# Kernel optimization log

Measured on AMD Instinct MI355X. Metric: run time of the kernel, lower is better.

Reference implementation:

```python
import jax, jax.numpy as jnp
import numpy as np

B, S, D, H, M = 4, 1024, 1024, 16, 128
HD = D // H  # 64


def setup_inputs() -> dict:
    key = jax.random.key(0)
    ks = jax.random.split(key, 12)
    s = 0.02
    return {
        "x": jax.random.normal(ks[0], (B, S, D), dtype=jnp.float32),
        "Wq": jax.random.normal(ks[1], (D, D), dtype=jnp.float32) * s,
        "bq": jnp.zeros((D,), dtype=jnp.float32),
        "Wk": jax.random.normal(ks[2], (D, D), dtype=jnp.float32) * s,
        "bk": jnp.zeros((D,), dtype=jnp.float32),
        "Wv": jax.random.normal(ks[3], (D, D), dtype=jnp.float32) * s,
        "bv": jnp.zeros((D,), dtype=jnp.float32),
        "Wo": jax.random.normal(ks[4], (D, D), dtype=jnp.float32) * s,
        "bo": jnp.zeros((D,), dtype=jnp.float32),
        "u": jax.random.normal(ks[5], (H, HD), dtype=jnp.float32) * s,
        "v": jax.random.normal(ks[6], (H, HD), dtype=jnp.float32) * s,
    }


def _rel_sinusoid_emb():
    # [2M+1, HD] sinusoidal embeddings over relative offsets -M..M
    rel_range = jnp.arange(-M, M + 1, dtype=jnp.float32)
    inv_freq = 1.0 / (10000.0 ** (jnp.arange(0, HD, 2, dtype=jnp.float32) / HD))
    sinusoid = rel_range[:, None] * inv_freq[None, :]  # [2M+1, HD/2]
    emb = jnp.zeros((2 * M + 1, HD), dtype=jnp.float32)
    emb = emb.at[:, 0::2].set(jnp.sin(sinusoid))
    emb = emb.at[:, 1::2].set(jnp.cos(sinusoid))
    return emb


def reference(x, Wq, bq, Wk, bk, Wv, bv, Wo, bo, u, v):
    scale = 1.0 / np.sqrt(HD).astype(np.float32)

    def heads(t):  # [B,S,D] -> [B,H,S,HD]
        return t.reshape(B, S, H, HD).transpose(0, 2, 1, 3)

    q = heads(x @ Wq + bq)
    k = heads(x @ Wk + bk)
    vv = heads(x @ Wv + bv)

    rel_emb = _rel_sinusoid_emb()  # [2M+1, HD]
    pos = jnp.arange(S)
    rel_index = jnp.clip(pos[None, :] - pos[:, None], -M, M) + M  # [S,S] int

    q_u = q + u[None, :, None, :]
    q_v = q + v[None, :, None, :]

    content = jnp.einsum("bhid,bhjd->bhij", q_u, k) * scale  # [B,H,S,S]
    # einsum('bhid,ijd->bhij', q_v, rel_emb[rel_index]) == gather of per-bucket scores
    rel_all = jnp.einsum("bhid,rd->bhir", q_v, rel_emb) * scale  # [B,H,S,2M+1]
    rel_scores = jnp.take_along_axis(rel_all, rel_index[None, None, :, :], axis=-1)

    attn = jax.nn.softmax(content + rel_scores, axis=-1)
    out = jnp.einsum("bhij,bhjd->bhid", attn, vv)  # [B,H,S,HD]
    out = out.transpose(0, 2, 1, 3).reshape(B, S, D)
    return out @ Wo + bo
```

## Files before the change

kernel.cpp:

```cpp
#include <hip/hip_runtime.h>
#include <math.h>


#define BB 4
#define SS 1024
#define DD 1024
#define HH 16
#define HDIM 64
#define SCALE 0.125f
#define KMAX_BOUND 16.0f

typedef __attribute__((ext_vector_type(8))) short short8;
typedef __attribute__((ext_vector_type(4))) float f32x4;
typedef __attribute__((ext_vector_type(4))) unsigned short us4;
typedef unsigned short u16;

#define MFMA __builtin_amdgcn_mfma_f32_16x16x32_bf16

__device__ __forceinline__ float b2f(u16 v) {
  return __uint_as_float((unsigned)v << 16);
}
__device__ __forceinline__ u16 f2b(float f) {
  unsigned u = __float_as_uint(f);
  return (u16)((u + 0x7FFF + ((u >> 16) & 1)) >> 16);
}
__device__ __forceinline__ void gl_lds16(const u16* g, u16* l) {
  __builtin_amdgcn_global_load_lds(
      (const __attribute__((address_space(1))) unsigned int*)(g),
      (__attribute__((address_space(3))) unsigned int*)(l), 16, 0, 0);
}

__global__ __launch_bounds__(256) void prep(
    const float* __restrict__ x,
    const float* __restrict__ W0, const float* __restrict__ W1,
    const float* __restrict__ W2, const float* __restrict__ W3,
    u16* __restrict__ xb,
    u16* __restrict__ T0, u16* __restrict__ T1,
    u16* __restrict__ T2, u16* __restrict__ T3,
    u16* __restrict__ Eb) {
  __shared__ float t[64 * 68];
  const int bid = blockIdx.x, tid = threadIdx.x;
  if (bid < 2048) {
    const size_t i = ((size_t)bid * 256 + tid) * 8;
    float4 a = *reinterpret_cast<const float4*>(&x[i]);
    float4 b = *reinterpret_cast<const float4*>(&x[i + 4]);
    short8 v;
    v[0] = (short)f2b(a.x); v[1] = (short)f2b(a.y);
    v[2] = (short)f2b(a.z); v[3] = (short)f2b(a.w);
    v[4] = (short)f2b(b.x); v[5] = (short)f2b(b.y);
    v[6] = (short)f2b(b.z); v[7] = (short)f2b(b.w);
    *reinterpret_cast<short8*>(&xb[i]) = v;
  } else if (bid < 3072) {
    const int wz = bid - 2048;
    const int z = wz >> 8;
    const float* W = z == 0 ? W0 : z == 1 ? W1 : z == 2 ? W2 : W3;
    u16* T = z == 0 ? T0 : z == 1 ? T1 : z == 2 ? T2 : T3;
    const int k0 = ((wz >> 4) & 15) * 64, n0 = (wz & 15) * 64;
#pragma unroll
    for (int rd = 0; rd < 4; ++rd) {
      const int idx = rd * 256 + tid;
      const int r = idx >> 4, c4 = (idx & 15) * 4;
      *reinterpret_cast<float4*>(&t[r * 68 + c4]) =
          *reinterpret_cast<const float4*>(&W[(size_t)(k0 + r) * DD + n0 + c4]);
    }
    __syncthreads();
#pragma unroll
    for (int rd = 0; rd < 2; ++rd) {
      const int idx = rd * 256 + tid;
      const int rr = idx >> 3, cc = (idx & 7) * 8;
      short8 v;
#pragma unroll
      for (int e = 0; e < 8; ++e) v[e] = (short)f2b(t[(cc + e) * 68 + rr]);
      *reinterpret_cast<short8*>(&T[(size_t)(n0 + rr) * DD + k0 + cc]) = v;
    }
  } else {
    const int j = (bid - 3072) * 4 + (tid >> 6);
    const int d = tid & 63;
    const int pair = d >> 1;
    const float inv_freq =
        exp2f(-((float)(2 * pair) / 64.0f) * 13.287712379549449f);
    const float arg = (float)j * inv_freq;
    const float val = (d & 1) ? cosf(arg) : sinf(arg);
    Eb[j * 64 + d] = f2b(val);
  }
}

__global__ __launch_bounds__(256, 3) void gemm_mfma(
    const u16* __restrict__ A,
    const u16* __restrict__ W0, const u16* __restrict__ W1, const u16* __restrict__ W2,
    const float* __restrict__ b0, const float* __restrict__ b1, const float* __restrict__ b2,
    void* o0, void* o1, void* o2, int final_mode) {
  const int z = blockIdx.z;
  const u16* Bt = z == 0 ? W0 : z == 1 ? W1 : W2;
  const float* bias = z == 0 ? b0 : z == 1 ? b1 : b2;
  __shared__ u16 As0[128 * 32];
  __shared__ u16 Bs0[128 * 32];
  __shared__ u16 As1[128 * 32];
  __shared__ u16 Bs1[128 * 32];
  const int tid = threadIdx.x;
  const int bm = blockIdx.y * 128, bn = blockIdx.x * 128;
  const int lane = tid & 63, w = tid >> 6;
  const int wr = w >> 1, wc = w & 1;
  const int lr = lane & 15, lg = lane >> 4;

  const int r_i0 = 32 * w + (lane >> 2);
  const int r_i1 = r_i0 + 16;
  const int q0 = (lane & 3) ^ ((r_i0 >> 1) & 3);
  const int q1 = (lane & 3) ^ ((r_i1 >> 1) & 3);
  const u16* gA0 = &A[(size_t)(bm + r_i0) * DD + q0 * 8];
  const u16* gA1 = &A[(size_t)(bm + r_i1) * DD + q1 * 8];
  const u16* gB0 = &Bt[(size_t)(bn + r_i0) * DD + q0 * 8];
  const u16* gB1 = &Bt[(size_t)(bn + r_i1) * DD + q1 * 8];
  const int lo0 = (32 * w) * 32;
  const int lo1 = (32 * w + 16) * 32;

  const f32x4 Z4 = {0.f, 0.f, 0.f, 0.f};
  f32x4 acc[4][4];
#pragma unroll
  for (int m = 0; m < 4; ++m)
#pragma unroll
    for (int n = 0; n < 4; ++n) acc[m][n] = Z4;

  auto STAGE = [&](u16* Ab, u16* Bb, int kk) {
    gl_lds16(gA0 + kk, Ab + lo0);
    gl_lds16(gA1 + kk, Ab + lo1);
    gl_lds16(gB0 + kk, Bb + lo0);
    gl_lds16(gB1 + kk, Bb + lo1);
  };
  auto COMPUTE = [&](u16* Ab, u16* Bb) {
    short8 af[4], bf[4];
#pragma unroll
    for (int m = 0; m < 4; ++m) {
      const int row = wr * 64 + m * 16 + lr;
      af[m] = *reinterpret_cast<short8*>(&Ab[row * 32 + ((lg ^ ((row >> 1) & 3)) * 8)]);
    }
#pragma unroll
    for (int n = 0; n < 4; ++n) {
      const int row = wc * 64 + n * 16 + lr;
      bf[n] = *reinterpret_cast<short8*>(&Bb[row * 32 + ((lg ^ ((row >> 1) & 3)) * 8)]);
    }
#pragma unroll
    for (int m = 0; m < 4; ++m)
#pragma unroll
      for (int n = 0; n < 4; ++n)
        acc[m][n] = MFMA(af[m], bf[n], acc[m][n], 0, 0, 0);
  };

  STAGE(As0, Bs0, 0);
  __syncthreads();
  for (int k0 = 0; k0 < DD; k0 += 64) {
    STAGE(As1, Bs1, k0 + 32);
    COMPUTE(As0, Bs0);
    __syncthreads();
    if (k0 + 64 < DD) STAGE(As0, Bs0, k0 + 64);
    COMPUTE(As1, Bs1);
    __syncthreads();
  }

  const int mode = final_mode ? 2 : (z == 2 ? 1 : 0);
  u16* ob = (u16*)(z == 0 ? o0 : z == 1 ? o1 : o2);
  float* of = (float*)o0;
#pragma unroll
  for (int m = 0; m < 4; ++m) {
#pragma unroll
    for (int n = 0; n < 4; ++n) {
      const int col = bn + wc * 64 + n * 16 + lr;
      const float bv = bias[col];
      const int row0 = bm + wr * 64 + m * 16 + lg * 4;
      if (mode == 0) {
#pragma unroll
        for (int g = 0; g < 4; ++g)
          ob[(size_t)(row0 + g) * DD + col] = f2b(acc[m][n][g] + bv);
      } else if (mode == 2) {
#pragma unroll
        for (int g = 0; g < 4; ++g)
          of[(size_t)(row0 + g) * DD + col] = acc[m][n][g] + bv;
      } else {
        const int bI = row0 >> 10, s0 = row0 & 1023;
        us4 pk;
#pragma unroll
        for (int g = 0; g < 4; ++g) pk[g] = f2b(acc[m][n][g] + bv);
        *reinterpret_cast<us4*>(&ob[(size_t)col * 4096 + bI * 1024 + s0]) = pk;
      }
    }
  }
}

__global__ __launch_bounds__(256, 2) void attn_mfma(
    const u16* __restrict__ Qg, const u16* __restrict__ Kg,
    const u16* __restrict__ Vtg, const u16* __restrict__ Eb,
    const float* __restrict__ ub, const float* __restrict__ vb,
    u16* __restrict__ AO) {
  __shared__ u16 kk0[64 * 128];
  __shared__ u16 kk1[64 * 128];
  __shared__ u16 vt0[64 * 64];
  __shared__ u16 vt1[64 * 64];
  __shared__ u16 ps_l[128 * 64];
  __shared__ float ls_l[128];

  const int tid = threadIdx.x;
  const int it = blockIdx.x, h = blockIdx.y, b = blockIdx.z;
  const int i0 = it * 128;
  const int lane = tid & 63, w = tid >> 6;
  const int lr = lane & 15, lg = lane >> 4;
  const f32x4 Z4 = {0.f, 0.f, 0.f, 0.f};
  auto needE = [&](int j0) { const int d = j0 - i0; return d >= -191 && d <= 255; };

  short8 aq[2][4];
  float bI[2], bL[2], bR[2];
#pragma unroll
  for (int m = 0; m < 2; ++m) {
    const int qpos = i0 + w * 32 + m * 16 + lr;
    const size_t qbase = (size_t)(b * SS + qpos) * DD + h * 64;
    const int iL = qpos >= 128 ? qpos - 128 : 0;
    const int iR = qpos <= 895 ? qpos + 128 : 1023;
    float nqu = 0.f, nqv = 0.f, clp = 0.f, crp = 0.f;
#pragma unroll
    for (int ks2 = 0; ks2 < 2; ++ks2) {
      const int d8 = ks2 * 32 + lg * 8;
      short8 q8 = *reinterpret_cast<const short8*>(&Qg[qbase + d8]);
      short8 e8 = *reinterpret_cast<const short8*>(&Eb[qpos * 64 + d8]);
      short8 eL8 = *reinterpret_cast<const short8*>(&Eb[iL * 64 + d8]);
      short8 eR8 = *reinterpret_cast<const short8*>(&Eb[iR * 64 + d8]);
      float us[8], vs[8];
      {
        float4 a = *reinterpret_cast<const float4*>(&ub[h * 64 + d8]);
        float4 d = *reinterpret_cast<const float4*>(&ub[h * 64 + d8 + 4]);
        us[0] = a.x; us[1] = a.y; us[2] = a.z; us[3] = a.w;
        us[4] = d.x; us[5] = d.y; us[6] = d.z; us[7] = d.w;
        float4 e = *reinterpret_cast<const float4*>(&vb[h * 64 + d8]);
        float4 f = *reinterpret_cast<const float4*>(&vb[h * 64 + d8 + 4]);
        vs[0] = e.x; vs[1] = e.y; vs[2] = e.z; vs[3] = e.w;
        vs[4] = f.x; vs[5] = f.y; vs[6] = f.z; vs[7] = f.w;
      }
      short8 xu, xr;
#pragma unroll
      for (int e = 0; e < 8; ++e) {
        const float qf = b2f((u16)q8[e]);
        xu[e] = (short)f2b(qf + us[e]);
        const float quf = b2f((u16)xu[e]);
        nqu = fmaf(quf, quf, nqu);
      }
#pragma unroll
      for (int p = 0; p < 4; ++p) {
        const float qv0 = b2f((u16)q8[2 * p]) + vs[2 * p];
        const float qv1 = b2f((u16)q8[2 * p + 1]) + vs[2 * p + 1];
        const float si = b2f((u16)e8[2 * p]), co = b2f((u16)e8[2 * p + 1]);
        const float r0 = qv0 * co + qv1 * si;
        const float r1 = qv1 * co - qv0 * si;
        xr[2 * p] = (short)f2b(r0);
        xr[2 * p + 1] = (short)f2b(r1);
        const float a0 = b2f((u16)xr[2 * p]), a1 = b2f((u16)xr[2 * p + 1]);
        nqv = fmaf(a0, a0, fmaf(a1, a1, nqv));
        clp = fmaf(a0, b2f((u16)eL8[2 * p]), fmaf(a1, b2f((u16)eL8[2 * p + 1]), clp));
        crp = fmaf(a0, b2f((u16)eR8[2 * p]), fmaf(a1, b2f((u16)eR8[2 * p + 1]), crp));
      }
      aq[m][ks2] = xu;
      aq[m][ks2 + 2] = xr;
    }
    nqu += __shfl_xor(nqu, 16); nqu += __shfl_xor(nqu, 32);
    nqv += __shfl_xor(nqv, 16); nqv += __shfl_xor(nqv, 32);
    clp += __shfl_xor(clp, 16); clp += __shfl_xor(clp, 32);
    crp += __shfl_xor(crp, 16); crp += __shfl_xor(crp, 32);
    const float Mrow =
        0.125f * KMAX_BOUND * sqrtf(nqu) + 0.7125f * sqrtf(nqv) + 0.03f;
    bI[m] = -Mrow;
    bL[m] = 0.125f * clp - Mrow;
    bR[m] = 0.125f * crp - Mrow;
  }

  float lsum[2] = {0.f, 0.f};
  f32x4 o_acc[2][4];
#pragma unroll
  for (int nq = 0; nq < 2; ++nq)
#pragma unroll
    for (int df = 0; df < 4; ++df) o_acc[nq][df] = Z4;

  const int srow = tid >> 2, sc4 = tid & 3;
  const int vr = tid >> 3, vc = tid & 7;
  const int rs = srow & 15;
  const size_t kcol = (size_t)h * 64 + sc4 * 16;

  short8 kA, kB, eA, eB, v0r, v1r;
  {
    const size_t kbase = (size_t)(b * SS + srow) * DD + kcol;
    kA = *reinterpret_cast<const short8*>(&Kg[kbase]);
    kB = *reinterpret_cast<const short8*>(&Kg[kbase + 8]);
    v0r = *reinterpret_cast<const short8*>(
        &Vtg[(size_t)(h * 64 + vr) * 4096 + b * SS + vc * 8]);
    v1r = *reinterpret_cast<const short8*>(
        &Vtg[(size_t)(h * 64 + vr + 32) * 4096 + b * SS + vc * 8]);
    *reinterpret_cast<short8*>(&kk0[srow * 128 + (((sc4 * 2) ^ rs) * 8)]) = kA;
    *reinterpret_cast<short8*>(&kk0[srow * 128 + (((sc4 * 2 + 1) ^ rs) * 8)]) = kB;
    if (needE(0)) {
      const size_t ebase = (size_t)srow * 64 + sc4 * 16;
      eA = *reinterpret_cast<const short8*>(&Eb[ebase]);
      eB = *reinterpret_cast<const short8*>(&Eb[ebase + 8]);
      *reinterpret_cast<short8*>(&kk0[srow * 128 + (((8 + sc4 * 2) ^ rs) * 8)]) = eA;
      *reinterpret_cast<short8*>(&kk0[srow * 128 + (((9 + sc4 * 2) ^ rs) * 8)]) = eB;
    }
    *reinterpret_cast<short8*>(&vt0[vr * 64 + ((vc ^ (vr & 7)) * 8)]) = v0r;
    *reinterpret_cast<short8*>(&vt0[(vr + 32) * 64 + ((vc ^ ((vr + 32) & 7)) * 8)]) = v1r;
  }
  __syncthreads();

  for (int jt = 0; jt < 16; ++jt) {
    const int j0 = jt * 64;
    u16* kk_l = (jt & 1) ? kk1 : kk0;
    u16* vt_l = (jt & 1) ? vt1 : vt0;
    u16* kk_n = (jt & 1) ? kk0 : kk1;
    u16* vt_n = (jt & 1) ? vt0 : vt1;
    const int jn = j0 + 64;

    if (jt < 15) {
      const size_t kbase = (size_t)(b * SS + jn + srow) * DD + kcol;
      kA = *reinterpret_cast<const short8*>(&Kg[kbase]);
      kB = *reinterpret_cast<const short8*>(&Kg[kbase + 8]);
      if (needE(jn)) {
        const size_t ebase = (size_t)(jn + srow) * 64 + sc4 * 16;
        eA = *reinterpret_cast<const short8*>(&Eb[ebase]);
        eB = *reinterpret_cast<const short8*>(&Eb[ebase + 8]);
      }
      v0r = *reinterpret_cast<const short8*>(
          &Vtg[(size_t)(h * 64 + vr) * 4096 + b * SS + jn + vc * 8]);
      v1r = *reinterpret_cast<const short8*>(
          &Vtg[(size_t)(h * 64 + vr + 32) * 4096 + b * SS + jn + vc * 8]);
    }

    const int roW = j0 - i0 - w * 32;
    if (roW < -191 || roW > 159) {
      const float fb0 = roW < 0 ? bL[0] : bR[0];
      const float fb1 = roW < 0 ? bL[1] : bR[1];
#pragma unroll
      for (int nf = 0; nf < 4; ++nf) {
        const int krow = nf * 16 + lr;
        short8 kf0 = *reinterpret_cast<short8*>(
            &kk_l[krow * 128 + ((lg ^ lr) * 8)]);
        short8 kf1 = *reinterpret_cast<short8*>(
            &kk_l[krow * 128 + (((4 + lg) ^ lr) * 8)]);
#pragma unroll
        for (int nq = 0; nq < 2; ++nq) {
          __builtin_amdgcn_s_setprio(1);
          f32x4 s = MFMA(kf0, aq[nq][0], Z4, 0, 0, 0);
          s = MFMA(kf1, aq[nq][1], s, 0, 0, 0);
          __builtin_amdgcn_s_setprio(0);
          const float base = nq == 0 ? fb0 : fb1;
          us4 pk;
#pragma unroll
          for (int g = 0; g < 4; ++g) {
            const float p = __expf(fmaf(s[g], SCALE, base));
            lsum[nq] += p;
            pk[g] = f2b(p);
          }
          const int prow = w * 32 + nq * 16 + lr;
          *reinterpret_cast<us4*>(
              &ps_l[prow * 64 + (((nf * 2 + (lg >> 1)) ^ (prow & 7)) * 8) +
                    4 * (lg & 1)]) = pk;
        }
      }
    } else {
#pragma unroll
      for (int nf = 0; nf < 4; ++nf) {
        const int krow = nf * 16 + lr;
        short8 kf0 = *reinterpret_cast<short8*>(
            &kk_l[krow * 128 + ((lg ^ lr) * 8)]);
        short8 kf1 = *reinterpret_cast<short8*>(
            &kk_l[krow * 128 + (((4 + lg) ^ lr) * 8)]);
        short8 kf2 = *reinterpret_cast<short8*>(
            &kk_l[krow * 128 + (((8 + lg) ^ lr) * 8)]);
        short8 kf3 = *reinterpret_cast<short8*>(
            &kk_l[krow * 128 + (((12 + lg) ^ lr) * 8)]);
#pragma unroll
        for (int nq = 0; nq < 2; ++nq) {
          __builtin_amdgcn_s_setprio(1);
          f32x4 c = MFMA(kf0, aq[nq][0], Z4, 0, 0, 0);
          c = MFMA(kf1, aq[nq][1], c, 0, 0, 0);
          f32x4 t = MFMA(kf2, aq[nq][2], c, 0, 0, 0);
          t = MFMA(kf3, aq[nq][3], t, 0, 0, 0);
          __builtin_amdgcn_s_setprio(0);
          const int rob = roW + nf * 16 + lg * 4 - nq * 16 - lr;
          us4 pk;
#pragma unroll
          for (int g = 0; g < 4; ++g) {
            const int ro = rob + g;
            const bool inr = (ro >= -128) && (ro <= 128);
            const float sval = inr ? t[g] : c[g];
            const float base = inr ? bI[nq] : (ro < -128 ? bL[nq] : bR[nq]);
            const float p = __expf(fmaf(sval, SCALE, base));
            lsum[nq] += p;
            pk[g] = f2b(p);
          }
          const int prow = w * 32 + nq * 16 + lr;
          *reinterpret_cast<us4*>(
              &ps_l[prow * 64 + (((nf * 2 + (lg >> 1)) ^ (prow & 7)) * 8) +
                    4 * (lg & 1)]) = pk;
        }
      }
    }

    __builtin_amdgcn_s_setprio(1);
#pragma unroll
    for (int ks = 0; ks < 2; ++ks) {
      short8 ap0, ap1;
      {
        const int r0q = w * 32 + lr;
        ap0 = *reinterpret_cast<short8*>(
            &ps_l[r0q * 64 + (((ks * 4 + lg) ^ (r0q & 7)) * 8)]);
        const int r1q = w * 32 + 16 + lr;
        ap1 = *reinterpret_cast<short8*>(
            &ps_l[r1q * 64 + (((ks * 4 + lg) ^ (r1q & 7)) * 8)]);
      }
#pragma unroll
      for (int df = 0; df < 4; ++df) {
        const int vrow = df * 16 + lr;
        short8 vf = *reinterpret_cast<short8*>(
            &vt_l[vrow * 64 + (((ks * 4 + lg) ^ (vrow & 7)) * 8)]);
        o_acc[0][df] = MFMA(ap0, vf, o_acc[0][df], 0, 0, 0);
        o_acc[1][df] = MFMA(ap1, vf, o_acc[1][df], 0, 0, 0);
      }
    }
    __builtin_amdgcn_s_setprio(0);

    if (jt < 15) {
      *reinterpret_cast<short8*>(&kk_n[srow * 128 + (((sc4 * 2) ^ rs) * 8)]) = kA;
      *reinterpret_cast<short8*>(&kk_n[srow * 128 + (((sc4 * 2 + 1) ^ rs) * 8)]) = kB;
      if (needE(jn)) {
        *reinterpret_cast<short8*>(&kk_n[srow * 128 + (((8 + sc4 * 2) ^ rs) * 8)]) = eA;
        *reinterpret_cast<short8*>(&kk_n[srow * 128 + (((9 + sc4 * 2) ^ rs) * 8)]) = eB;
      }
      *reinterpret_cast<short8*>(&vt_n[vr * 64 + ((vc ^ (vr & 7)) * 8)]) = v0r;
      *reinterpret_cast<short8*>(&vt_n[(vr + 32) * 64 + ((vc ^ ((vr + 32) & 7)) * 8)]) = v1r;
      __syncthreads();
    }
  }

#pragma unroll
  for (int nq = 0; nq < 2; ++nq) {
    lsum[nq] += __shfl_xor(lsum[nq], 16);
    lsum[nq] += __shfl_xor(lsum[nq], 32);
    ls_l[w * 32 + nq * 16 + lr] = lsum[nq];
  }
  __syncthreads();
#pragma unroll
  for (int nq = 0; nq < 2; ++nq) {
#pragma unroll
    for (int g = 0; g < 4; ++g) {
      const float inv = 1.0f / ls_l[w * 32 + nq * 16 + lg * 4 + g];
      const int row = b * SS + i0 + w * 32 + nq * 16 + lg * 4 + g;
#pragma unroll
      for (int df = 0; df < 4; ++df) {
        AO[(size_t)row * DD + h * 64 + df * 16 + lr] =
            f2b(o_acc[nq][df][g] * inv);
      }
    }
  }
}

extern "C" void kernel_launch(void* const* d_in, const int* in_sizes, int n_in,
                              void* d_out, int out_size, void* d_ws, size_t ws_size,
                              hipStream_t stream) {
  const float* x  = (const float*)d_in[0];
  const float* Wq = (const float*)d_in[1];
  const float* bq = (const float*)d_in[2];
  const float* Wk = (const float*)d_in[3];
  const float* bk = (const float*)d_in[4];
  const float* Wv = (const float*)d_in[5];
  const float* bv = (const float*)d_in[6];
  const float* Wo = (const float*)d_in[7];
  const float* bo = (const float*)d_in[8];
  const float* u  = (const float*)d_in[9];
  const float* v  = (const float*)d_in[10];
  float* out = (float*)d_out;

  char* p = (char*)d_ws;
  const size_t TOK = (size_t)4096 * 1024 * 2;
  const size_t WSZ = (size_t)1024 * 1024 * 2;
  u16* Eb   = (u16*)p; p += (size_t)1024 * 64 * 2;
  u16* xb   = (u16*)p; p += TOK;
  u16* Wqt  = (u16*)p; p += WSZ;
  u16* Wkt  = (u16*)p; p += WSZ;
  u16* Wvt  = (u16*)p; p += WSZ;
  u16* Wot  = (u16*)p; p += WSZ;
  u16* Qb   = (u16*)p; p += TOK;
  u16* Kb   = (u16*)p; p += TOK;
  u16* Vt   = (u16*)p; p += TOK;
  u16* AOb  = (u16*)p; p += TOK;

  prep<<<3328, 256, 0, stream>>>(x, Wq, Wk, Wv, Wo, xb, Wqt, Wkt, Wvt, Wot, Eb);

  gemm_mfma<<<dim3(8, 32, 3), 256, 0, stream>>>(
      xb, Wqt, Wkt, Wvt, bq, bk, bv, Qb, Kb, Vt, 0);

  attn_mfma<<<dim3(SS / 128, HH, BB), 256, 0, stream>>>(
      Qb, Kb, Vt, Eb, u, v, AOb);

  gemm_mfma<<<dim3(8, 32, 1), 256, 0, stream>>>(
      AOb, Wot, Wot, Wot, bo, bo, bo, out, out, out, 1);
}
```

Before: 107.5 us.

## Split attention block warps 2x2 over query and key halves with reduction

Changes the warp decomposition in the attention kernel from each warp owning 32 query rows across all 64 keys to a 2x2 grid. Each warp now owns 64 query rows and a 32-key half of each tile, so every K fragment read from shared memory feeds four query fragments instead of two. Partial row sums and output accumulators from the two key-half warps are combined at the end through shared memory, reusing the K buffers as scratch. The aim is fewer LDS fragment reads per MFMA, at the cost of doubled accumulator registers (o_acc 4x4, aq 4x4), which may reduce occupancy under launch_bounds(256,2), plus an extra reduction pass.

```diff
diff --git a/kernel.cpp b/kernel.cpp
--- a/kernel.cpp
+++ b/kernel.cpp
@@ -196,21 +196,22 @@
   __shared__ u16 vt0[64 * 64];
   __shared__ u16 vt1[64 * 64];
   __shared__ u16 ps_l[128 * 64];
-  __shared__ float ls_l[128];
+  __shared__ float ls_l[2 * 128];
 
   const int tid = threadIdx.x;
   const int it = blockIdx.x, h = blockIdx.y, b = blockIdx.z;
   const int i0 = it * 128;
   const int lane = tid & 63, w = tid >> 6;
   const int lr = lane & 15, lg = lane >> 4;
+  const int qh = w >> 1, kh = w & 1;
   const f32x4 Z4 = {0.f, 0.f, 0.f, 0.f};
   auto needE = [&](int j0) { const int d = j0 - i0; return d >= -191 && d <= 255; };
 
-  short8 aq[2][4];
-  float bI[2], bL[2], bR[2];
-#pragma unroll
-  for (int m = 0; m < 2; ++m) {
-    const int qpos = i0 + w * 32 + m * 16 + lr;
+  short8 aq[4][4];
+  float bI[4], bL[4], bR[4];
+#pragma unroll
+  for (int m = 0; m < 4; ++m) {
+    const int qpos = i0 + qh * 64 + m * 16 + lr;
     const size_t qbase = (size_t)(b * SS + qpos) * DD + h * 64;
     const int iL = qpos >= 128 ? qpos - 128 : 0;
     const int iR = qpos <= 895 ? qpos + 128 : 1023;
@@ -269,12 +270,12 @@
     bR[m] = 0.125f * crp - Mrow;
   }
 
-  float lsum[2] = {0.f, 0.f};
-  f32x4 o_acc[2][4];
-#pragma unroll
-  for (int nq = 0; nq < 2; ++nq)
-#pragma unroll
-    for (int df = 0; df < 4; ++df) o_acc[nq][df] = Z4;
+  float lsum[4] = {0.f, 0.f, 0.f, 0.f};
+  f32x4 o_acc[4][4];
+#pragma unroll
+  for (int m = 0; m < 4; ++m)
+#pragma unroll
+    for (int df = 0; df < 4; ++df) o_acc[m][df] = Z4;
 
   const int srow = tid >> 2, sc4 = tid & 3;
   const int vr = tid >> 3, vc = tid & 7;
@@ -327,41 +328,40 @@
           &Vtg[(size_t)(h * 64 + vr + 32) * 4096 + b * SS + jn + vc * 8]);
     }
 
-    const int roW = j0 - i0 - w * 32;
-    if (roW < -191 || roW > 159) {
-      const float fb0 = roW < 0 ? bL[0] : bR[0];
-      const float fb1 = roW < 0 ? bL[1] : bR[1];
-#pragma unroll
-      for (int nf = 0; nf < 4; ++nf) {
-        const int krow = nf * 16 + lr;
+    const int roW = j0 + kh * 32 - i0 - qh * 64;
+    const int prow_base = qh * 64 + lr;
+    if (roW < -159 || roW > 191) {
+#pragma unroll
+      for (int nf = 0; nf < 2; ++nf) {
+        const int krow = kh * 32 + nf * 16 + lr;
         short8 kf0 = *reinterpret_cast<short8*>(
             &kk_l[krow * 128 + ((lg ^ lr) * 8)]);
         short8 kf1 = *reinterpret_cast<short8*>(
             &kk_l[krow * 128 + (((4 + lg) ^ lr) * 8)]);
 #pragma unroll
-        for (int nq = 0; nq < 2; ++nq) {
+        for (int m = 0; m < 4; ++m) {
           __builtin_amdgcn_s_setprio(1);
-          f32x4 s = MFMA(kf0, aq[nq][0], Z4, 0, 0, 0);
-          s = MFMA(kf1, aq[nq][1], s, 0, 0, 0);
+          f32x4 s = MFMA(kf0, aq[m][0], Z4, 0, 0, 0);
+          s = MFMA(kf1, aq[m][1], s, 0, 0, 0);
           __builtin_amdgcn_s_setprio(0);
-          const float base = nq == 0 ? fb0 : fb1;
+          const float base = roW < 0 ? bL[m] : bR[m];
           us4 pk;
 #pragma unroll
           for (int g = 0; g < 4; ++g) {
             const float p = __expf(fmaf(s[g], SCALE, base));
-            lsum[nq] += p;
+            lsum[m] += p;
             pk[g] = f2b(p);
           }
-          const int prow = w * 32 + nq * 16 + lr;
+          const int prow = prow_base + m * 16;
+          const int c8 = kh * 4 + nf * 2 + (lg >> 1);
           *reinterpret_cast<us4*>(
-              &ps_l[prow * 64 + (((nf * 2 + (lg >> 1)) ^ (prow & 7)) * 8) +
-                    4 * (lg & 1)]) = pk;
+              &ps_l[prow * 64 + ((c8 ^ (prow & 7)) * 8) + 4 * (lg & 1)]) = pk;
         }
       }
     } else {
 #pragma unroll
-      for (int nf = 0; nf < 4; ++nf) {
-        const int krow = nf * 16 + lr;
+      for (int nf = 0; nf < 2; ++nf) {
+        const int krow = kh * 32 + nf * 16 + lr;
         short8 kf0 = *reinterpret_cast<short8*>(
             &kk_l[krow * 128 + ((lg ^ lr) * 8)]);
         short8 kf1 = *reinterpret_cast<short8*>(
@@ -371,52 +371,45 @@
         short8 kf3 = *reinterpret_cast<short8*>(
             &kk_l[krow * 128 + (((12 + lg) ^ lr) * 8)]);
 #pragma unroll
-        for (int nq = 0; nq < 2; ++nq) {
+        for (int m = 0; m < 4; ++m) {
           __builtin_amdgcn_s_setprio(1);
-          f32x4 c = MFMA(kf0, aq[nq][0], Z4, 0, 0, 0);
-          c = MFMA(kf1, aq[nq][1], c, 0, 0, 0);
-          f32x4 t = MFMA(kf2, aq[nq][2], c, 0, 0, 0);
-          t = MFMA(kf3, aq[nq][3], t, 0, 0, 0);
+          f32x4 c = MFMA(kf0, aq[m][0], Z4, 0, 0, 0);
+          c = MFMA(kf1, aq[m][1], c, 0, 0, 0);
+          f32x4 t = MFMA(kf2, aq[m][2], c, 0, 0, 0);
+          t = MFMA(kf3, aq[m][3], t, 0, 0, 0);
           __builtin_amdgcn_s_setprio(0);
-          const int rob = roW + nf * 16 + lg * 4 - nq * 16 - lr;
+          const int rob = roW + nf * 16 + lg * 4 - m * 16 - lr;
           us4 pk;
 #pragma unroll
           for (int g = 0; g < 4; ++g) {
             const int ro = rob + g;
             const bool inr = (ro >= -128) && (ro <= 128);
             const float sval = inr ? t[g] : c[g];
-            const float base = inr ? bI[nq] : (ro < -128 ? bL[nq] : bR[nq]);
+            const float base = inr ? bI[m] : (ro < -128 ? bL[m] : bR[m]);
             const float p = __expf(fmaf(sval, SCALE, base));
-            lsum[nq] += p;
+            lsum[m] += p;
             pk[g] = f2b(p);
           }
-          const int prow = w * 32 + nq * 16 + lr;
+          const int prow = prow_base + m * 16;
+          const int c8 = kh * 4 + nf * 2 + (lg >> 1);
           *reinterpret_cast<us4*>(
-              &ps_l[prow * 64 + (((nf * 2 + (lg >> 1)) ^ (prow & 7)) * 8) +
-                    4 * (lg & 1)]) = pk;
+              &ps_l[prow * 64 + ((c8 ^ (prow & 7)) * 8) + 4 * (lg & 1)]) = pk;
         }
       }
     }
 
     __builtin_amdgcn_s_setprio(1);
 #pragma unroll
-    for (int ks = 0; ks < 2; ++ks) {
-      short8 ap0, ap1;
-      {
-        const int r0q = w * 32 + lr;
-        ap0 = *reinterpret_cast<short8*>(
-            &ps_l[r0q * 64 + (((ks * 4 + lg) ^ (r0q & 7)) * 8)]);
-        const int r1q = w * 32 + 16 + lr;
-        ap1 = *reinterpret_cast<short8*>(
-            &ps_l[r1q * 64 + (((ks * 4 + lg) ^ (r1q & 7)) * 8)]);
-      }
+    for (int m2 = 0; m2 < 4; ++m2) {
+      const int arow = prow_base + m2 * 16;
+      short8 ap = *reinterpret_cast<short8*>(
+          &ps_l[arow * 64 + (((kh * 4 + lg) ^ (arow & 7)) * 8)]);
 #pragma unroll
       for (int df = 0; df < 4; ++df) {
         const int vrow = df * 16 + lr;
         short8 vf = *reinterpret_cast<short8*>(
-            &vt_l[vrow * 64 + (((ks * 4 + lg) ^ (vrow & 7)) * 8)]);
-        o_acc[0][df] = MFMA(ap0, vf, o_acc[0][df], 0, 0, 0);
-        o_acc[1][df] = MFMA(ap1, vf, o_acc[1][df], 0, 0, 0);
+            &vt_l[vrow * 64 + (((kh * 4 + lg) ^ (vrow & 7)) * 8)]);
+        o_acc[m2][df] = MFMA(ap, vf, o_acc[m2][df], 0, 0, 0);
       }
     }
     __builtin_amdgcn_s_setprio(0);
@@ -435,22 +428,43 @@
   }
 
 #pragma unroll
-  for (int nq = 0; nq < 2; ++nq) {
-    lsum[nq] += __shfl_xor(lsum[nq], 16);
-    lsum[nq] += __shfl_xor(lsum[nq], 32);
-    ls_l[w * 32 + nq * 16 + lr] = lsum[nq];
+  for (int m = 0; m < 4; ++m) {
+    lsum[m] += __shfl_xor(lsum[m], 16);
+    lsum[m] += __shfl_xor(lsum[m], 32);
+  }
+  if (lg == 0) {
+#pragma unroll
+    for (int m = 0; m < 4; ++m)
+      ls_l[kh * 128 + qh * 64 + m * 16 + lr] = lsum[m];
   }
   __syncthreads();
-#pragma unroll
-  for (int nq = 0; nq < 2; ++nq) {
-#pragma unroll
-    for (int g = 0; g < 4; ++g) {
-      const float inv = 1.0f / ls_l[w * 32 + nq * 16 + lg * 4 + g];
-      const int row = b * SS + i0 + w * 32 + nq * 16 + lg * 4 + g;
-#pragma unroll
-      for (int df = 0; df < 4; ++df) {
-        AO[(size_t)row * DD + h * 64 + df * 16 + lr] =
-            f2b(o_acc[nq][df][g] * inv);
+  if (kh == 1) {
+    float* sc = (float*)(qh ? kk1 : kk0);
+#pragma unroll
+    for (int m2 = 0; m2 < 4; ++m2)
+#pragma unroll
+      for (int df = 0; df < 4; ++df)
+#pragma unroll
+        for (int g = 0; g < 4; ++g)
+          sc[(m2 * 16 + lg * 4 + g) * 64 + df * 16 + lr] = o_acc[m2][df][g];
+  }
+  __syncthreads();
+  if (kh == 0) {
+    const float* sc = (const float*)(qh ? kk1 : kk0);
+#pragma unroll
+    for (int m2 = 0; m2 < 4; ++m2) {
+#pragma unroll
+      for (int g = 0; g < 4; ++g) {
+        const int rl = m2 * 16 + lg * 4 + g;
+        const float l =
+            ls_l[qh * 64 + rl] + ls_l[128 + qh * 64 + rl];
+        const float inv = 1.0f / l;
+        const int row = b * SS + i0 + qh * 64 + rl;
+#pragma unroll
+        for (int df = 0; df < 4; ++df) {
+          AO[(size_t)row * DD + h * 64 + df * 16 + lr] =
+              f2b((o_acc[m2][df][g] + sc[rl * 64 + df * 16 + lr]) * inv);
+        }
       }
     }
   }
```

After: 112.8 us. 4.9% more time.
